# Optimization experiments

Measured on AMD Instinct MI355X. Metric: run time of the kernel, lower is better.

## Reference

```python
import jax, jax.numpy as jnp
import numpy as np

T, B, I, H, L = 1024, 64, 512, 512, 2


def _gru_layer(x_seq, h0, w_ih, w_hh, b_ih, b_hh):
    # x_seq: [T, B, in], h0: [B, H]
    # Precompute input-side gates for all timesteps in one big GEMM.
    gx = jnp.einsum('tbi,gi->tbg', x_seq, w_ih) + b_ih  # [T, B, 3H]

    def step(h, gx_t):
        gh = h @ w_hh.T + b_hh                 # [B, 3H]
        i_r, i_z, i_n = jnp.split(gx_t, 3, axis=-1)
        h_r, h_z, h_n = jnp.split(gh, 3, axis=-1)
        r = jax.nn.sigmoid(i_r + h_r)
        z = jax.nn.sigmoid(i_z + h_z)
        n = jnp.tanh(i_n + r * h_n)
        hy = n + z * (h - n)                   # newgate + inputgate*(hx - newgate)
        return hy, hy

    hT, out = jax.lax.scan(step, h0, gx)
    return out, hT  # out: [T, B, H]


def setup_inputs() -> dict:
    key = jax.random.key(0)
    ks = jax.random.split(key, 10)
    stdv = 1.0 / np.sqrt(H)
    u = lambda k, shp: jax.random.uniform(k, shp, jnp.float32, -stdv, stdv)
    return {
        'x': jax.random.normal(ks[0], (T, B, I), jnp.float32),
        'hx': jax.random.normal(ks[1], (L, B, H), jnp.float32),
        'w_ih_0': u(ks[2], (3 * H, I)),
        'w_hh_0': u(ks[3], (3 * H, H)),
        'b_ih_0': u(ks[4], (3 * H,)),
        'b_hh_0': u(ks[5], (3 * H,)),
        'w_ih_1': u(ks[6], (3 * H, H)),
        'w_hh_1': u(ks[7], (3 * H, H)),
        'b_ih_1': u(ks[8], (3 * H,)),
        'b_hh_1': u(ks[9], (3 * H,)),
    }


def reference(x, hx, w_ih_0, w_hh_0, b_ih_0, b_hh_0, w_ih_1, w_hh_1, b_ih_1, b_hh_1):
    out0, h0T = _gru_layer(x, hx[0], w_ih_0, w_hh_0, b_ih_0, b_hh_0)
    out1, h1T = _gru_layer(out0, hx[1], w_ih_1, w_hh_1, b_ih_1, b_hh_1)
    output = out1                         # [T, B, H] (batch_first=False)
    output_hs = jnp.stack([h0T, h1T], 0)  # [L, B, H]
    return output, output_hs
```

## Files before the change

### kernel.cpp

```cpp
#include <hip/hip_runtime.h>
#include <cstdint>
#include <cstddef>

#define T_N 1024
#define B_N 64
#define I_N 512
#define H_N 512
#define G3  (3*H_N)
#define NBLK 256

typedef _Float16 f16;
typedef _Float16 f16x2 __attribute__((ext_vector_type(2)));
typedef unsigned long long ull;

#define SLOT(d) (((d)+2)&1)
#define TAG1(d) ((((d)+2)>>1)&1)

__device__ __forceinline__ f16x2 mkh2(float a, float b) {
  f16x2 v; v.x = (_Float16)a; v.y = (_Float16)b; return v;
}
__device__ __forceinline__ f16x2 bch2(unsigned int u) {
  return __builtin_bit_cast(f16x2, u);
}
__device__ __forceinline__ float fdot2_(f16x2 a, f16x2 b, float c) {
#if __has_builtin(__builtin_amdgcn_fdot2)
  return __builtin_amdgcn_fdot2(a, b, c, false);
#else
  return fmaf((float)a.x, (float)b.x, fmaf((float)a.y, (float)b.y, c));
#endif
}
__device__ __forceinline__ float sigm_(float x) { return 1.f / (1.f + __expf(-x)); }
__device__ __forceinline__ float tanhf_(float x) {
  float xx = fminf(15.f, fmaxf(-15.f, x));
  float e = __expf(2.f * xx);
  return (e - 1.f) / (e + 1.f);
}

__global__ __launch_bounds__(256) void gemm_nt(
    const float* __restrict__ A,
    const float* __restrict__ W,
    const float* __restrict__ bias,
    float* __restrict__ C,
    int M, int N, int K)
{
  __shared__ float As[32][68];
  __shared__ float Ws[32][68];
  const int tid = threadIdx.x;
  const int n0 = blockIdx.x * 64;
  const int m0 = blockIdx.y * 64;
  const int ty = tid >> 4;
  const int tx = tid & 15;

  float acc[4][4];
#pragma unroll
  for (int i = 0; i < 4; ++i)
#pragma unroll
    for (int jj = 0; jj < 4; ++jj) acc[i][jj] = 0.f;

  for (int k0 = 0; k0 < K; k0 += 32) {
#pragma unroll
    for (int i = 0; i < 2; ++i) {
      int idx = tid + i * 256;
      int r   = idx >> 3;
      int c4  = idx & 7;
      float4 va = *(const float4*)(A + (size_t)(m0 + r) * K + k0 + c4 * 4);
      As[c4*4+0][r] = va.x; As[c4*4+1][r] = va.y;
      As[c4*4+2][r] = va.z; As[c4*4+3][r] = va.w;
      float4 vw = *(const float4*)(W + (size_t)(n0 + r) * K + k0 + c4 * 4);
      Ws[c4*4+0][r] = vw.x; Ws[c4*4+1][r] = vw.y;
      Ws[c4*4+2][r] = vw.z; Ws[c4*4+3][r] = vw.w;
    }
    __syncthreads();
#pragma unroll
    for (int k = 0; k < 32; ++k) {
      float4 a = *(const float4*)&As[k][ty * 4];
      float4 w = *(const float4*)&Ws[k][tx * 4];
      acc[0][0] += a.x*w.x; acc[0][1] += a.x*w.y; acc[0][2] += a.x*w.z; acc[0][3] += a.x*w.w;
      acc[1][0] += a.y*w.x; acc[1][1] += a.y*w.y; acc[1][2] += a.y*w.z; acc[1][3] += a.y*w.w;
      acc[2][0] += a.z*w.x; acc[2][1] += a.z*w.y; acc[2][2] += a.z*w.z; acc[2][3] += a.z*w.w;
      acc[3][0] += a.w*w.x; acc[3][1] += a.w*w.y; acc[3][2] += a.w*w.z; acc[3][3] += a.w*w.w;
    }
    __syncthreads();
  }

  float4 bv = *(const float4*)(bias + n0 + tx * 4);
#pragma unroll
  for (int i = 0; i < 4; ++i) {
    int row = m0 + ty * 4 + i;
    float4 o;
    o.x = acc[i][0] + bv.x; o.y = acc[i][1] + bv.y;
    o.z = acc[i][2] + bv.z; o.w = acc[i][3] + bv.w;
    *(float4*)(C + (size_t)row * N + n0 + tx * 4) = o;
  }
}

__global__ __launch_bounds__(256) void pack_h_init(
    const float* __restrict__ hx, f16* h0x, f16* h1x)
{
  int i = blockIdx.x * 256 + threadIdx.x;
  unsigned short a = __builtin_bit_cast(unsigned short, (f16)hx[i]) & 0xFFFEu;
  unsigned short b = __builtin_bit_cast(unsigned short, (f16)hx[B_N * H_N + i]) & 0xFFFEu;
  ((unsigned short*)h0x)[B_N * H_N + i] = a;
  ((unsigned short*)h1x)[B_N * H_N + i] = b;
}

#define D4(acc, wv, vv)                      \
  acc = fdot2_(wv[0], bch2((vv).x), acc);    \
  acc = fdot2_(wv[1], bch2((vv).y), acc);    \
  acc = fdot2_(wv[2], bch2((vv).z), acc);    \
  acc = fdot2_(wv[3], bch2((vv).w), acc);

__global__ __launch_bounds__(256, 1) void gru_fused(
    const float* __restrict__ gx,
    const float* __restrict__ hx,
    const float* wih1, const float* whh0, const float* whh1,
    const float* bih1, const float* bhh0, const float* bhh1,
    float* __restrict__ out,
    float* __restrict__ hT,
    f16* h0x, f16* h1x)
{
  __shared__ __align__(16) ull sh0q[1024];
  __shared__ __align__(16) ull sh1q[1024];
  __shared__ float red[(384 + 512) * 20];
  __shared__ __align__(8) unsigned short pkA[128], pkB[128];

  const int tid = threadIdx.x;
  const int bid = blockIdx.x;
  const int g = bid & 7;
  const int j = bid >> 3;
  const int u = tid >> 4;
  const int s = tid & 15;
  const ull M = 0x0001000100010001ULL;

  f16x2 wA[3][4][4], wX[3][4][4], wH[3][4][4];
#pragma unroll
  for (int q = 0; q < 3; ++q) {
    const size_t row = (size_t)(q * H_N + 16 * j + u) * H_N;
    const float* pA = whh0 + row;
    const float* pX = wih1 + row;
    const float* pH = whh1 + row;
#pragma unroll
    for (int c = 0; c < 4; ++c)
#pragma unroll
      for (int d = 0; d < 4; ++d) {
        const int k = 8 * s + 128 * c + 2 * d;
        wA[q][c][d] = mkh2(pA[k], pA[k + 1]);
        wX[q][c][d] = mkh2(pX[k], pX[k + 1]);
        wH[q][c][d] = mkh2(pH[k], pH[k + 1]);
      }
  }

  const int gl = tid & 127, gu = gl & 15, gb8 = gl >> 4;
  const bool isA = tid < 128;
  const int unit = 16 * j + gu, gbi = 8 * g + gb8;
  const float bRv = isA ? bhh0[unit]           : (bih1[unit] + bhh1[unit]);
  const float bZv = isA ? bhh0[H_N + unit]     : (bih1[H_N + unit] + bhh1[H_N + unit]);
  const float bNv = isA ? bhh0[2 * H_N + unit] : bih1[2 * H_N + unit];
  const float bDv = isA ? 0.f                  : bhh1[2 * H_N + unit];
  float hv = hx[(size_t)(isA ? 0 : B_N * H_N) + (size_t)gbi * H_N + unit];

  for (int t = 0; t <= T_N; ++t) {
    const bool runA = (t < T_N), runB = (t > 0);

    float ir0 = 0, iz0 = 0, in0 = 0;
    if (runA && isA) {
      const float* p = gx + ((size_t)t * B_N + gbi) * G3 + unit;
      ir0 = p[0]; iz0 = p[H_N]; in0 = p[2 * H_N];
    }

    const ull* s0 = (const ull*)h0x + (size_t)SLOT(t - 1) * 8192 + (size_t)(8 * g) * 128;
    const ull* s1 = (const ull*)h1x + (size_t)SLOT(t - 2) * 8192 + (size_t)(8 * g) * 128;
    const ull e0 = TAG1(t - 1) ? M : 0ULL;
    const ull e1 = TAG1(t - 2) ? M : 0ULL;
    ull v0[4], v1[4];
    bool k0[4] = {false, false, false, false};
    bool k1[4] = {!runB, !runB, !runB, !runB};
    for (;;) {
#pragma unroll
      for (int e = 0; e < 4; ++e) {
        if (!k0[e]) v0[e] = __hip_atomic_load(s0 + e * 256 + tid, __ATOMIC_RELAXED, __HIP_MEMORY_SCOPE_AGENT);
        if (!k1[e]) v1[e] = __hip_atomic_load(s1 + e * 256 + tid, __ATOMIC_RELAXED, __HIP_MEMORY_SCOPE_AGENT);
      }
      bool all = true;
#pragma unroll
      for (int e = 0; e < 4; ++e) {
        if (!k0[e]) k0[e] = ((v0[e] & M) == e0);
        if (!k1[e]) k1[e] = ((v1[e] & M) == e1);
        all = all && k0[e] && k1[e];
      }
      if (__all(all)) break;
      __builtin_amdgcn_s_sleep(1);
    }
#pragma unroll
    for (int e = 0; e < 4; ++e) {
      sh0q[e * 256 + tid] = v0[e];
      if (runB) sh1q[e * 256 + tid] = v1[e];
    }
    __syncthreads();

    float aA[3][8], aB[4][8];
#pragma unroll
    for (int q = 0; q < 3; ++q)
#pragma unroll
      for (int bb = 0; bb < 8; ++bb) aA[q][bb] = 0.f;
#pragma unroll
    for (int q = 0; q < 4; ++q)
#pragma unroll
      for (int bb = 0; bb < 8; ++bb) aB[q][bb] = 0.f;

    const uint4* x4 = (const uint4*)sh0q;
    const uint4* h4 = (const uint4*)sh1q;
#pragma unroll
    for (int bb = 0; bb < 8; ++bb) {
      uint4 xc[4], hc[4];
#pragma unroll
      for (int c = 0; c < 4; ++c) xc[c] = x4[bb * 64 + s + 16 * c];
      if (runB) {
#pragma unroll
        for (int c = 0; c < 4; ++c) hc[c] = h4[bb * 64 + s + 16 * c];
      }
      if (runA) {
#pragma unroll
        for (int q = 0; q < 3; ++q) {
          float a = aA[q][bb];
#pragma unroll
          for (int c = 0; c < 4; ++c) { D4(a, wA[q][c], xc[c]); }
          aA[q][bb] = a;
        }
      }
      if (runB) {
        float a0 = aB[0][bb], a1 = aB[1][bb], a2 = aB[2][bb], a3 = aB[3][bb];
#pragma unroll
        for (int c = 0; c < 4; ++c) {
          D4(a0, wX[0][c], xc[c]); D4(a0, wH[0][c], hc[c]);
          D4(a1, wX[1][c], xc[c]); D4(a1, wH[1][c], hc[c]);
          D4(a2, wX[2][c], xc[c]);
          D4(a3, wH[2][c], hc[c]);
        }
        aB[0][bb] = a0; aB[1][bb] = a1; aB[2][bb] = a2; aB[3][bb] = a3;
      }
    }

    const int col = (s + u) & 15;
    if (runA) {
#pragma unroll
      for (int q = 0; q < 3; ++q)
#pragma unroll
        for (int bb = 0; bb < 8; ++bb)
          red[(size_t)(u + 16 * (q * 8 + bb)) * 20 + col] = aA[q][bb];
    }
    if (runB) {
#pragma unroll
      for (int q = 0; q < 4; ++q)
#pragma unroll
        for (int bb = 0; bb < 8; ++bb)
          red[(size_t)(384 + u + 16 * (q * 8 + bb)) * 20 + col] = aB[q][bb];
    }
    __syncthreads();

    if (isA) {
      if (runA) {
        float sg[3];
#pragma unroll
        for (int q = 0; q < 3; ++q) {
          const float* rp = &red[(size_t)(gu + 16 * (q * 8 + gb8)) * 20];
          float4 a = *(const float4*)rp,        b4 = *(const float4*)(rp + 4);
          float4 c4 = *(const float4*)(rp + 8), d4 = *(const float4*)(rp + 12);
          sg[q] = (((a.x + a.y) + (a.z + a.w)) + ((b4.x + b4.y) + (b4.z + b4.w)))
                + (((c4.x + c4.y) + (c4.z + c4.w)) + ((d4.x + d4.y) + (d4.z + d4.w)));
        }
        float r = sigm_(ir0 + sg[0] + bRv);
        float z = sigm_(iz0 + sg[1] + bZv);
        float n = tanhf_(in0 + r * (sg[2] + bNv));
        float hy = n + z * (hv - n); hv = hy;
        pkA[gl] = __builtin_bit_cast(unsigned short, (f16)hy);
        if (t == T_N - 1) hT[(size_t)gbi * H_N + unit] = hy;
      }
    } else {
      if (runB) {
        float sg[4];
#pragma unroll
        for (int q = 0; q < 4; ++q) {
          const float* rp = &red[(size_t)(384 + gu + 16 * (q * 8 + gb8)) * 20];
          float4 a = *(const float4*)rp,        b4 = *(const float4*)(rp + 4);
          float4 c4 = *(const float4*)(rp + 8), d4 = *(const float4*)(rp + 12);
          sg[q] = (((a.x + a.y) + (a.z + a.w)) + ((b4.x + b4.y) + (b4.z + b4.w)))
                + (((c4.x + c4.y) + (c4.z + c4.w)) + ((d4.x + d4.y) + (d4.z + d4.w)));
        }
        float r = sigm_(sg[0] + bRv);
        float z = sigm_(sg[1] + bZv);
        float n = tanhf_(sg[2] + bNv + r * (sg[3] + bDv));
        float hy = n + z * (hv - n); hv = hy;
        pkB[gl] = __builtin_bit_cast(unsigned short, (f16)hy);
        out[((size_t)(t - 1) * B_N + gbi) * H_N + unit] = hy;
        if (t == T_N) hT[(size_t)(B_N + gbi) * H_N + unit] = hy;
      }
    }
    __syncthreads();

    if (tid < 32) {
      if (runA) {
        ull v = ((const ull*)pkA)[tid];
        v = (v & ~M) | (TAG1(t) ? M : 0ULL);
        ull* dp = (ull*)h0x + (size_t)SLOT(t) * 8192
                + (size_t)(8 * g + (tid >> 2)) * 128 + 4 * j + (tid & 3);
        __hip_atomic_store(dp, v, __ATOMIC_RELAXED, __HIP_MEMORY_SCOPE_AGENT);
      }
    } else if (tid < 64) {
      if (runB) {
        const int l = tid - 32;
        ull v = ((const ull*)pkB)[l];
        v = (v & ~M) | (TAG1(t - 1) ? M : 0ULL);
        ull* dp = (ull*)h1x + (size_t)SLOT(t - 1) * 8192
                + (size_t)(8 * g + (l >> 2)) * 128 + 4 * j + (l & 3);
        __hip_atomic_store(dp, v, __ATOMIC_RELAXED, __HIP_MEMORY_SCOPE_AGENT);
      }
    }
  }
}

extern "C" void kernel_launch(void* const* d_in, const int* in_sizes, int n_in,
                              void* d_out, int out_size, void* d_ws, size_t ws_size,
                              hipStream_t stream)
{
  const float* x    = (const float*)d_in[0];
  const float* hx   = (const float*)d_in[1];
  const float* wih0 = (const float*)d_in[2];
  const float* whh0 = (const float*)d_in[3];
  const float* bih0 = (const float*)d_in[4];
  const float* bhh0 = (const float*)d_in[5];
  const float* wih1 = (const float*)d_in[6];
  const float* whh1 = (const float*)d_in[7];
  const float* bih1 = (const float*)d_in[8];
  const float* bhh1 = (const float*)d_in[9];
  float* out = (float*)d_out;

  float* gxb = (float*)d_ws;
  f16*   h0x = (f16*)(gxb + (size_t)T_N * B_N * G3);
  f16*   h1x = h0x + 2 * B_N * H_N;

  pack_h_init<<<128, 256, 0, stream>>>(hx, h0x, h1x);

  dim3 gg(G3 / 64, (T_N * B_N) / 64);
  gemm_nt<<<gg, 256, 0, stream>>>(x, wih0, bih0, gxb, T_N * B_N, G3, I_N);

  gru_fused<<<NBLK, 256, 0, stream>>>(gxb, hx, wih1, whh0, whh1,
                                      bih1, bhh0, bhh1,
                                      out, out + (size_t)T_N * B_N * H_N,
                                      h0x, h1x);
}
```

Baseline: 8.998 ms.

## Skew layer-1 by two steps and overlap its compute with layer-0 polling

```diff
diff --git a/kernel.cpp b/kernel.cpp
--- a/kernel.cpp
+++ b/kernel.cpp
@@ -110,6 +110,31 @@
   acc = fdot2_(wv[2], bch2((vv).z), acc);    \
   acc = fdot2_(wv[3], bch2((vv).w), acc);
 
+template <int NQ>
+__device__ __forceinline__ void rscat8(float a[][8], float* r, int s) {
+#pragma unroll
+  for (int q = 0; q < NQ; ++q) {
+    float k4[4];
+#pragma unroll
+    for (int i = 0; i < 4; ++i) {
+      float snd = (s & 1) ? a[q][i] : a[q][4 + i];
+      float kp  = (s & 1) ? a[q][4 + i] : a[q][i];
+      k4[i] = kp + __shfl_xor(snd, 1);
+    }
+    float k2[2];
+#pragma unroll
+    for (int i = 0; i < 2; ++i) {
+      float snd = (s & 2) ? k4[i] : k4[2 + i];
+      float kp  = (s & 2) ? k4[2 + i] : k4[i];
+      k2[i] = kp + __shfl_xor(snd, 2);
+    }
+    float snd = (s & 4) ? k2[0] : k2[1];
+    float kp  = (s & 4) ? k2[1] : k2[0];
+    float k1 = kp + __shfl_xor(snd, 4);
+    r[q] = k1 + __shfl_xor(k1, 8);
+  }
+}
+
 __global__ __launch_bounds__(256, 1) void gru_fused(
     const float* __restrict__ gx,
     const float* __restrict__ hx,
@@ -119,9 +144,8 @@
     float* __restrict__ hT,
     f16* h0x, f16* h1x)
 {
-  __shared__ __align__(16) ull sh0q[1024];
+  __shared__ __align__(16) ull sh0q[2][1024];
   __shared__ __align__(16) ull sh1q[1024];
-  __shared__ float red[(384 + 512) * 20];
   __shared__ __align__(8) unsigned short pkA[128], pkB[128];
 
   const int tid = threadIdx.x;
@@ -150,86 +174,79 @@
       }
   }
 
-  const int gl = tid & 127, gu = gl & 15, gb8 = gl >> 4;
-  const bool isA = tid < 128;
-  const int unit = 16 * j + gu, gbi = 8 * g + gb8;
-  const float bRv = isA ? bhh0[unit]           : (bih1[unit] + bhh1[unit]);
-  const float bZv = isA ? bhh0[H_N + unit]     : (bih1[H_N + unit] + bhh1[H_N + unit]);
-  const float bNv = isA ? bhh0[2 * H_N + unit] : bih1[2 * H_N + unit];
-  const float bDv = isA ? 0.f                  : bhh1[2 * H_N + unit];
-  float hv = hx[(size_t)(isA ? 0 : B_N * H_N) + (size_t)gbi * H_N + unit];
-
-  for (int t = 0; t <= T_N; ++t) {
-    const bool runA = (t < T_N), runB = (t > 0);
+  const int bb   = 4 * (s & 1) + 2 * ((s >> 1) & 1) + ((s >> 2) & 1);
+  const int unit = 16 * j + u;
+  const int gbi  = 8 * g + bb;
+  const float bR0 = bhh0[unit], bZ0 = bhh0[H_N + unit], bN0 = bhh0[2 * H_N + unit];
+  const float bR1 = bih1[unit] + bhh1[unit];
+  const float bZ1 = bih1[H_N + unit] + bhh1[H_N + unit];
+  const float bN1x = bih1[2 * H_N + unit], bN1h = bhh1[2 * H_N + unit];
+  float hv0 = hx[(size_t)gbi * H_N + unit];
+  float hv1 = hx[(size_t)(B_N + gbi) * H_N + unit];
+
+  for (int t = 0; t <= T_N + 1; ++t) {
+    const bool runA = (t < T_N);
+    const bool pollH0 = (t <= T_N);
+    const bool runB = (t >= 2);
+    const int cur = t & 1;
+
+    const ull* s0 = (const ull*)h0x + (size_t)SLOT(t - 1) * 8192 + (size_t)(8 * g) * 128;
+    const ull* s1 = (const ull*)h1x + (size_t)SLOT(t - 3) * 8192 + (size_t)(8 * g) * 128;
+    const ull e0 = TAG1(t - 1) ? M : 0ULL;
+    const ull e1 = TAG1(t - 3) ? M : 0ULL;
+    ull v0[4], v1[4];
+    bool k0[4] = {false, false, false, false};
+    if (pollH0) {
+#pragma unroll
+      for (int e = 0; e < 4; ++e)
+        v0[e] = __hip_atomic_load(s0 + e * 256 + tid, __ATOMIC_RELAXED, __HIP_MEMORY_SCOPE_AGENT);
+    }
+    if (runB) {
+#pragma unroll
+      for (int e = 0; e < 4; ++e)
+        v1[e] = __hip_atomic_load(s1 + e * 256 + tid, __ATOMIC_RELAXED, __HIP_MEMORY_SCOPE_AGENT);
+    }
 
     float ir0 = 0, iz0 = 0, in0 = 0;
-    if (runA && isA) {
+    if (runA) {
       const float* p = gx + ((size_t)t * B_N + gbi) * G3 + unit;
       ir0 = p[0]; iz0 = p[H_N]; in0 = p[2 * H_N];
     }
 
-    const ull* s0 = (const ull*)h0x + (size_t)SLOT(t - 1) * 8192 + (size_t)(8 * g) * 128;
-    const ull* s1 = (const ull*)h1x + (size_t)SLOT(t - 2) * 8192 + (size_t)(8 * g) * 128;
-    const ull e0 = TAG1(t - 1) ? M : 0ULL;
-    const ull e1 = TAG1(t - 2) ? M : 0ULL;
-    ull v0[4], v1[4];
-    bool k0[4] = {false, false, false, false};
-    bool k1[4] = {!runB, !runB, !runB, !runB};
-    for (;;) {
-#pragma unroll
-      for (int e = 0; e < 4; ++e) {
-        if (!k0[e]) v0[e] = __hip_atomic_load(s0 + e * 256 + tid, __ATOMIC_RELAXED, __HIP_MEMORY_SCOPE_AGENT);
-        if (!k1[e]) v1[e] = __hip_atomic_load(s1 + e * 256 + tid, __ATOMIC_RELAXED, __HIP_MEMORY_SCOPE_AGENT);
-      }
-      bool all = true;
-#pragma unroll
-      for (int e = 0; e < 4; ++e) {
-        if (!k0[e]) k0[e] = ((v0[e] & M) == e0);
-        if (!k1[e]) k1[e] = ((v1[e] & M) == e1);
-        all = all && k0[e] && k1[e];
-      }
-      if (__all(all)) break;
-      __builtin_amdgcn_s_sleep(1);
-    }
-#pragma unroll
-    for (int e = 0; e < 4; ++e) {
-      sh0q[e * 256 + tid] = v0[e];
-      if (runB) sh1q[e * 256 + tid] = v1[e];
-    }
-    __syncthreads();
-
-    float aA[3][8], aB[4][8];
-#pragma unroll
-    for (int q = 0; q < 3; ++q)
-#pragma unroll
-      for (int bb = 0; bb < 8; ++bb) aA[q][bb] = 0.f;
-#pragma unroll
-    for (int q = 0; q < 4; ++q)
-#pragma unroll
-      for (int bb = 0; bb < 8; ++bb) aB[q][bb] = 0.f;
-
-    const uint4* x4 = (const uint4*)sh0q;
-    const uint4* h4 = (const uint4*)sh1q;
-#pragma unroll
-    for (int bb = 0; bb < 8; ++bb) {
-      uint4 xc[4], hc[4];
-#pragma unroll
-      for (int c = 0; c < 4; ++c) xc[c] = x4[bb * 64 + s + 16 * c];
-      if (runB) {
-#pragma unroll
-        for (int c = 0; c < 4; ++c) hc[c] = h4[bb * 64 + s + 16 * c];
-      }
-      if (runA) {
-#pragma unroll
-        for (int q = 0; q < 3; ++q) {
-          float a = aA[q][bb];
-#pragma unroll
-          for (int c = 0; c < 4; ++c) { D4(a, wA[q][c], xc[c]); }
-          aA[q][bb] = a;
-        }
-      }
-      if (runB) {
-        float a0 = aB[0][bb], a1 = aB[1][bb], a2 = aB[2][bb], a3 = aB[3][bb];
+    if (runB) {
+      bool k1[4] = {false, false, false, false};
+      for (;;) {
+        bool all = true;
+#pragma unroll
+        for (int e = 0; e < 4; ++e) {
+          if (!k1[e]) k1[e] = ((v1[e] & M) == e1);
+          all = all && k1[e];
+        }
+        if (__all(all)) break;
+        __builtin_amdgcn_s_sleep(1);
+#pragma unroll
+        for (int e = 0; e < 4; ++e)
+          if (!k1[e]) v1[e] = __hip_atomic_load(s1 + e * 256 + tid, __ATOMIC_RELAXED, __HIP_MEMORY_SCOPE_AGENT);
+      }
+#pragma unroll
+      for (int e = 0; e < 4; ++e) sh1q[e * 256 + tid] = v1[e];
+    }
+    __syncthreads();
+
+    if (runB) {
+      float aB[4][8];
+#pragma unroll
+      for (int q = 0; q < 4; ++q)
+#pragma unroll
+        for (int b8 = 0; b8 < 8; ++b8) aB[q][b8] = 0.f;
+      const uint4* xp = (const uint4*)sh0q[cur ^ 1];
+      const uint4* hp = (const uint4*)sh1q;
+#pragma unroll
+      for (int b8 = 0; b8 < 8; ++b8) {
+        uint4 xc[4], hc[4];
+#pragma unroll
+        for (int c = 0; c < 4; ++c) { xc[c] = xp[b8 * 64 + s + 16 * c]; hc[c] = hp[b8 * 64 + s + 16 * c]; }
+        float a0 = aB[0][b8], a1 = aB[1][b8], a2 = aB[2][b8], a3 = aB[3][b8];
 #pragma unroll
         for (int c = 0; c < 4; ++c) {
           D4(a0, wX[0][c], xc[c]); D4(a0, wH[0][c], hc[c]);
@@ -237,63 +254,66 @@
           D4(a2, wX[2][c], xc[c]);
           D4(a3, wH[2][c], hc[c]);
         }
-        aB[0][bb] = a0; aB[1][bb] = a1; aB[2][bb] = a2; aB[3][bb] = a3;
-      }
-    }
-
-    const int col = (s + u) & 15;
+        aB[0][b8] = a0; aB[1][b8] = a1; aB[2][b8] = a2; aB[3][b8] = a3;
+      }
+      float rB[4];
+      rscat8<4>(aB, rB, s);
+      float r = sigm_(rB[0] + bR1);
+      float z = sigm_(rB[1] + bZ1);
+      float n = tanhf_(rB[2] + bN1x + r * (rB[3] + bN1h));
+      float hy = n + z * (hv1 - n); hv1 = hy;
+      if (s < 8) pkB[bb * 16 + u] = __builtin_bit_cast(unsigned short, (f16)hy);
+    }
+
+    if (pollH0) {
+      for (;;) {
+        bool all = true;
+#pragma unroll
+        for (int e = 0; e < 4; ++e) {
+          if (!k0[e]) k0[e] = ((v0[e] & M) == e0);
+          all = all && k0[e];
+        }
+        if (__all(all)) break;
+        __builtin_amdgcn_s_sleep(1);
+#pragma unroll
+        for (int e = 0; e < 4; ++e)
+          if (!k0[e]) v0[e] = __hip_atomic_load(s0 + e * 256 + tid, __ATOMIC_RELAXED, __HIP_MEMORY_SCOPE_AGENT);
+      }
+#pragma unroll
+      for (int e = 0; e < 4; ++e) sh0q[cur][e * 256 + tid] = v0[e];
+    }
+    __syncthreads();
+
     if (runA) {
+      float aA[3][8];
 #pragma unroll
       for (int q = 0; q < 3; ++q)
 #pragma unroll
-        for (int bb = 0; bb < 8; ++bb)
-          red[(size_t)(u + 16 * (q * 8 + bb)) * 20 + col] = aA[q][bb];
-    }
-    if (runB) {
-#pragma unroll
-      for (int q = 0; q < 4; ++q)
-#pragma unroll
-        for (int bb = 0; bb < 8; ++bb)
-          red[(size_t)(384 + u + 16 * (q * 8 + bb)) * 20 + col] = aB[q][bb];
-    }
-    __syncthreads();
-
-    if (isA) {
-      if (runA) {
-        float sg[3];
-#pragma unroll
-        for (int q = 0; q < 3; ++q) {
-          const float* rp = &red[(size_t)(gu + 16 * (q * 8 + gb8)) * 20];
-          float4 a = *(const float4*)rp,        b4 = *(const float4*)(rp + 4);
-          float4 c4 = *(const float4*)(rp + 8), d4 = *(const float4*)(rp + 12);
-          sg[q] = (((a.x + a.y) + (a.z + a.w)) + ((b4.x + b4.y) + (b4.z + b4.w)))
-                + (((c4.x + c4.y) + (c4.z + c4.w)) + ((d4.x + d4.y) + (d4.z + d4.w)));
-        }
-        float r = sigm_(ir0 + sg[0] + bRv);
-        float z = sigm_(iz0 + sg[1] + bZv);
-        float n = tanhf_(in0 + r * (sg[2] + bNv));
-        float hy = n + z * (hv - n); hv = hy;
-        pkA[gl] = __builtin_bit_cast(unsigned short, (f16)hy);
+        for (int b8 = 0; b8 < 8; ++b8) aA[q][b8] = 0.f;
+      const uint4* xp = (const uint4*)sh0q[cur];
+#pragma unroll
+      for (int b8 = 0; b8 < 8; ++b8) {
+        uint4 xc[4];
+#pragma unroll
+        for (int c = 0; c < 4; ++c) xc[c] = xp[b8 * 64 + s + 16 * c];
+        float a0 = aA[0][b8], a1 = aA[1][b8], a2 = aA[2][b8];
+#pragma unroll
+        for (int c = 0; c < 4; ++c) {
+          D4(a0, wA[0][c], xc[c]);
+          D4(a1, wA[1][c], xc[c]);
+          D4(a2, wA[2][c], xc[c]);
+        }
+        aA[0][b8] = a0; aA[1][b8] = a1; aA[2][b8] = a2;
+      }
+      float rA[3];
+      rscat8<3>(aA, rA, s);
+      float r = sigm_(ir0 + rA[0] + bR0);
+      float z = sigm_(iz0 + rA[1] + bZ0);
+      float n = tanhf_(in0 + r * (rA[2] + bN0));
+      float hy = n + z * (hv0 - n); hv0 = hy;
+      if (s < 8) {
+        pkA[bb * 16 + u] = __builtin_bit_cast(unsigned short, (f16)hy);
         if (t == T_N - 1) hT[(size_t)gbi * H_N + unit] = hy;
-      }
-    } else {
-      if (runB) {
-        float sg[4];
-#pragma unroll
-        for (int q = 0; q < 4; ++q) {
-          const float* rp = &red[(size_t)(384 + gu + 16 * (q * 8 + gb8)) * 20];
-          float4 a = *(const float4*)rp,        b4 = *(const float4*)(rp + 4);
-          float4 c4 = *(const float4*)(rp + 8), d4 = *(const float4*)(rp + 12);
-          sg[q] = (((a.x + a.y) + (a.z + a.w)) + ((b4.x + b4.y) + (b4.z + b4.w)))
-                + (((c4.x + c4.y) + (c4.z + c4.w)) + ((d4.x + d4.y) + (d4.z + d4.w)));
-        }
-        float r = sigm_(sg[0] + bRv);
-        float z = sigm_(sg[1] + bZv);
-        float n = tanhf_(sg[2] + bNv + r * (sg[3] + bDv));
-        float hy = n + z * (hv - n); hv = hy;
-        pkB[gl] = __builtin_bit_cast(unsigned short, (f16)hy);
-        out[((size_t)(t - 1) * B_N + gbi) * H_N + unit] = hy;
-        if (t == T_N) hT[(size_t)(B_N + gbi) * H_N + unit] = hy;
       }
     }
     __syncthreads();
@@ -310,10 +330,18 @@
       if (runB) {
         const int l = tid - 32;
         ull v = ((const ull*)pkB)[l];
-        v = (v & ~M) | (TAG1(t - 1) ? M : 0ULL);
-        ull* dp = (ull*)h1x + (size_t)SLOT(t - 1) * 8192
-                + (size_t)(8 * g + (l >> 2)) * 128 + 4 * j + (l & 3);
-        __hip_atomic_store(dp, v, __ATOMIC_RELAXED, __HIP_MEMORY_SCOPE_AGENT);
+        f16x2 p0 = bch2((unsigned int)v), p1 = bch2((unsigned int)(v >> 32));
+        float4 o = {(float)p0.x, (float)p0.y, (float)p1.x, (float)p1.y};
+        float* op = out + ((size_t)(t - 2) * B_N + 8 * g + (l >> 2)) * H_N + 16 * j + 4 * (l & 3);
+        *(float4*)op = o;
+        if (t == T_N + 1)
+          *(float4*)(hT + (size_t)(B_N + 8 * g + (l >> 2)) * H_N + 16 * j + 4 * (l & 3)) = o;
+        if (t <= T_N) {
+          v = (v & ~M) | (TAG1(t - 2) ? M : 0ULL);
+          ull* dp = (ull*)h1x + (size_t)SLOT(t - 2) * 8192
+                  + (size_t)(8 * g + (l >> 2)) * 128 + 4 * j + (l & 3);
+          __hip_atomic_store(dp, v, __ATOMIC_RELAXED, __HIP_MEMORY_SCOPE_AGENT);
+        }
       }
     }
   }
```

Result: slower. 10.42 ms (+15.9%).
